# Kernel optimization log

Hardware: AMD Instinct MI355X
Metric: run time of the kernel (lower is better)

The kernel has to match this reference:

```python
import jax, jax.numpy as jnp
import numpy as np

B, S, D = 1, 2048, 4096
H, KVH, HD = 32, 8, 128
GROUPS = H // KVH  # 4
SCALE = HD ** -0.5
NEG = jnp.finfo(jnp.float32).min


def rotate_half(x):
    x1 = x[..., : x.shape[-1] // 2]
    x2 = x[..., x.shape[-1] // 2:]
    return jnp.concatenate((-x2, x1), axis=-1)


def setup_inputs() -> dict:
    key = jax.random.key(0)
    ks = jax.random.split(key, 8)
    return {
        "hidden_states": jax.random.normal(ks[0], (B, S, D), dtype=jnp.float32),
        "cos": jax.random.uniform(ks[1], (B, S, HD), dtype=jnp.float32),
        "sin": jax.random.uniform(ks[2], (B, S, HD), dtype=jnp.float32),
        "attention_mask": jnp.ones((B, S), dtype=bool),
        "wq": jax.random.normal(ks[3], (D, H * HD), dtype=jnp.float32) * 0.02,
        "wk": jax.random.normal(ks[4], (D, KVH * HD), dtype=jnp.float32) * 0.02,
        "wv": jax.random.normal(ks[5], (D, KVH * HD), dtype=jnp.float32) * 0.02,
        "wo": jax.random.normal(ks[6], (H * HD, D), dtype=jnp.float32) * 0.02,
    }


def reference(hidden_states, cos, sin, attention_mask, wq, wk, wv, wo):
    b, s, _ = hidden_states.shape
    # projections -> (B,S,heads,head_dim)
    q = (hidden_states @ wq).reshape(b, s, H, HD)
    k = (hidden_states @ wk).reshape(b, s, KVH, HD)
    v = (hidden_states @ wv).reshape(b, s, KVH, HD)
    # RoPE (cos/sin unsqueezed at head axis)
    c = cos[:, :, None, :]
    si = sin[:, :, None, :]
    q = q * c + rotate_half(q) * si
    k = k * c + rotate_half(k) * si
    # GQA: repeat kv heads (cache_index=0, max_len==S -> cache write is identity)
    k = jnp.repeat(k, GROUPS, axis=2)
    v = jnp.repeat(v, GROUPS, axis=2)
    # mask: causal AND padding; bias 0 / -inf
    causal = jnp.tril(jnp.ones((s, s), dtype=bool))[None, None]  # (1,1,S,S)
    mask = causal & attention_mask[:, None, None, :]  # (B,1,S,S)
    bias = jnp.where(mask, 0.0, NEG).astype(hidden_states.dtype)
    # scores (B,H,S,S)
    scores = jnp.einsum("bqhd,bkhd->bhqk", q, k) * SCALE + bias
    attn = jax.nn.softmax(scores, axis=-1)
    out = jnp.einsum("bhqk,bkhd->bqhd", attn, v).reshape(b, s, H * HD)
    return out @ wo
```

## Files before the change

### kernel.cpp

```cpp
#include <hip/hip_runtime.h>
#include <hip/hip_bf16.h>

#define SEQ   2048
#define DM    4096
#define NH    32
#define NKVH  8
#define HD    128
#define NQKV  6144
#define KOFF  4096
#define VOFF  5120
#define QLD   5120
#define SCALE 0.08838834764831845f

typedef __attribute__((ext_vector_type(4))) float f32x4;
typedef __attribute__((ext_vector_type(8))) short short8;

__device__ __forceinline__ unsigned short f2bf(float f) {
  union { float f; unsigned int u; } v; v.f = f;
  unsigned int r = v.u + 0x7FFF + ((v.u >> 16) & 1);
  return (unsigned short)(r >> 16);
}
__device__ __forceinline__ float bf2f(unsigned short b) {
  union { unsigned int u; float f; } v; v.u = ((unsigned int)b) << 16;
  return v.f;
}

__device__ __forceinline__ void gld16(const unsigned short* g, unsigned short* l) {
  __builtin_amdgcn_global_load_lds(
      (const __attribute__((address_space(1))) unsigned int*)g,
      (__attribute__((address_space(3))) unsigned int*)l, 16, 0, 0);
}

__global__ __launch_bounds__(256) void prep(const float* __restrict__ hs,
                                            const float* __restrict__ wq,
                                            const float* __restrict__ wk,
                                            const float* __restrict__ wv,
                                            const float* __restrict__ wo,
                                            unsigned short* __restrict__ hsb,
                                            unsigned short* __restrict__ wqkvT,
                                            unsigned short* __restrict__ woT) {
  __shared__ unsigned short t2[64][72];
  const int bxg = blockIdx.x;
  const int tid = threadIdx.x;
  if (bxg < 8192) {
    size_t i = ((size_t)bxg * 256 + tid) * 4;
    float4 v = *(const float4*)(hs + i);
    ushort4 o;
    o.x = f2bf(v.x); o.y = f2bf(v.y); o.z = f2bf(v.z); o.w = f2bf(v.w);
    *(ushort4*)(hsb + i) = o;
    return;
  }
  const int b  = bxg - 8192;
  const int bx = b % 160;
  const int k0 = (b / 160) * 64;
  const float* W; unsigned short* out; int N, n0, row_off;
  if (bx < 64)      { W = wq; out = wqkvT; N = 4096; n0 = bx * 64;        row_off = 0;    }
  else if (bx < 80) { W = wk; out = wqkvT; N = 1024; n0 = (bx - 64) * 64; row_off = 4096; }
  else if (bx < 96) { W = wv; out = wqkvT; N = 1024; n0 = (bx - 80) * 64; row_off = 5120; }
  else              { W = wo; out = woT;   N = 4096; n0 = (bx - 96) * 64; row_off = 0;    }

  const int n  = tid & 63;
  const int q  = tid >> 6;
#pragma unroll
  for (int i = 0; i < 4; ++i) {
    const int kq = (i * 4 + q) * 4;
    float f0 = W[(size_t)(k0 + kq + 0) * N + n0 + n];
    float f1 = W[(size_t)(k0 + kq + 1) * N + n0 + n];
    float f2 = W[(size_t)(k0 + kq + 2) * N + n0 + n];
    float f3 = W[(size_t)(k0 + kq + 3) * N + n0 + n];
    ushort4 u; u.x = f2bf(f0); u.y = f2bf(f1); u.z = f2bf(f2); u.w = f2bf(f3);
    *(ushort4*)&t2[n][kq] = u;
  }
  __syncthreads();

  const int sn = tid >> 3;
  const int c8 = (tid & 7) * 8;
#pragma unroll
  for (int i = 0; i < 2; ++i) {
    const int nn = sn + i * 32;
    short8 v = *(const short8*)&t2[nn][c8];
    *(short8*)&out[(size_t)(row_off + n0 + nn) * DM + k0 + c8] = v;
  }
}

__global__ __launch_bounds__(256) void gemm_bt(const unsigned short* __restrict__ A,
                                               const unsigned short* __restrict__ Bt,
                                               void* __restrict__ C,
                                               unsigned short* __restrict__ vt,
                                               int M, int N, int K, int ldc, int c_fp32) {
  __shared__ unsigned short As[2][128 * 32];
  __shared__ unsigned short Bs[2][128 * 32];
  const int tid  = threadIdx.x;
  const int m0   = blockIdx.y * 128;
  const int n0   = blockIdx.x * 128;
  const int w    = tid >> 6;
  const int lane = tid & 63;
  const int l16  = lane & 15;
  const int quad = lane >> 4;
  const int wr   = (w >> 1) * 64;
  const int wc   = (w & 1) * 64;

  f32x4 acc[4][4];
#pragma unroll
  for (int i = 0; i < 4; ++i)
#pragma unroll
    for (int j = 0; j < 4; ++j) acc[i][j] = (f32x4){0.f, 0.f, 0.f, 0.f};

  const int sr  = lane >> 2;
  const int pb  = lane & 3;
  const int sws = (sr & 3) ^ ((sr >> 2) & 3);
  const int kb  = ((pb ^ sws) << 3);
  const unsigned short* ga0 = A  + (size_t)(m0 + w * 16 + sr) * K + kb;
  const unsigned short* ga1 = A  + (size_t)(m0 + 64 + w * 16 + sr) * K + kb;
  const unsigned short* gb0 = Bt + (size_t)(n0 + w * 16 + sr) * K + kb;
  const unsigned short* gb1 = Bt + (size_t)(n0 + 64 + w * 16 + sr) * K + kb;
  const int lofs0 = (w * 16) * 32;
  const int lofs1 = (64 + w * 16) * 32;

  const int swf  = (l16 & 3) ^ ((l16 >> 2) & 3);
  const int fcol = ((quad ^ swf) << 3);

  gld16(ga0, &As[0][lofs0]);
  gld16(ga1, &As[0][lofs1]);
  gld16(gb0, &Bs[0][lofs0]);
  gld16(gb1, &Bs[0][lofs1]);

  int p = 0;
  for (int k0 = 0; k0 < K; k0 += 32) {
    __syncthreads();
    if (k0 + 32 < K) {
      gld16(ga0 + k0 + 32, &As[p ^ 1][lofs0]);
      gld16(ga1 + k0 + 32, &As[p ^ 1][lofs1]);
      gld16(gb0 + k0 + 32, &Bs[p ^ 1][lofs0]);
      gld16(gb1 + k0 + 32, &Bs[p ^ 1][lofs1]);
    }
    short8 af[4], bfr[4];
#pragma unroll
    for (int mt = 0; mt < 4; ++mt)
      af[mt] = *(const short8*)&As[p][(wr + mt * 16 + l16) * 32 + fcol];
#pragma unroll
    for (int nt = 0; nt < 4; ++nt)
      bfr[nt] = *(const short8*)&Bs[p][(wc + nt * 16 + l16) * 32 + fcol];
#pragma unroll
    for (int mt = 0; mt < 4; ++mt)
#pragma unroll
      for (int nt = 0; nt < 4; ++nt)
        acc[mt][nt] = __builtin_amdgcn_mfma_f32_16x16x32_bf16(af[mt], bfr[nt], acc[mt][nt], 0, 0, 0);
    p ^= 1;
  }

  if (vt && n0 >= VOFF) {
#pragma unroll
    for (int mt = 0; mt < 4; ++mt)
#pragma unroll
      for (int nt = 0; nt < 4; ++nt) {
        int col  = (n0 - VOFF) + wc + nt * 16 + l16;
        int row0 = m0 + wr + mt * 16 + quad * 4;
        ushort4 ov;
        ov.x = f2bf(acc[mt][nt][0]); ov.y = f2bf(acc[mt][nt][1]);
        ov.z = f2bf(acc[mt][nt][2]); ov.w = f2bf(acc[mt][nt][3]);
        *(ushort4*)&vt[(size_t)col * SEQ + row0] = ov;
      }
  } else if (c_fp32) {
    float* Cf = (float*)C;
#pragma unroll
    for (int mt = 0; mt < 4; ++mt)
#pragma unroll
      for (int nt = 0; nt < 4; ++nt) {
        int col = n0 + wc + nt * 16 + l16;
#pragma unroll
        for (int r = 0; r < 4; ++r)
          Cf[(size_t)(m0 + wr + mt * 16 + quad * 4 + r) * ldc + col] = acc[mt][nt][r];
      }
  } else {
    unsigned short* Cb = (unsigned short*)C;
#pragma unroll
    for (int mt = 0; mt < 4; ++mt)
#pragma unroll
      for (int nt = 0; nt < 4; ++nt) {
        int col = n0 + wc + nt * 16 + l16;
#pragma unroll
        for (int r = 0; r < 4; ++r)
          Cb[(size_t)(m0 + wr + mt * 16 + quad * 4 + r) * ldc + col] = f2bf(acc[mt][nt][r]);
      }
  }
}

__global__ __launch_bounds__(256) void rope_kernel(unsigned short* __restrict__ QKV,
                                                   const float* __restrict__ cosb,
                                                   const float* __restrict__ sinb) {
  int idx = blockIdx.x * 256 + threadIdx.x;
  int i = idx & 63;
  int h = (idx >> 6) % 40;
  int s = idx / 2560;
  size_t base = (size_t)s * QLD + (size_t)h * 128;
  float q1 = bf2f(QKV[base + i]);
  float q2 = bf2f(QKV[base + i + 64]);
  float c1 = cosb[s * 128 + i],      s1 = sinb[s * 128 + i];
  float c2 = cosb[s * 128 + i + 64], s2 = sinb[s * 128 + i + 64];
  QKV[base + i]      = f2bf(q1 * c1 - q2 * s1);
  QKV[base + i + 64] = f2bf(q2 * c2 + q1 * s2);
}

__global__ __launch_bounds__(256) void flash_attn(const unsigned short* __restrict__ QKV,
                                                  const unsigned short* __restrict__ Vt_g,
                                                  unsigned short* __restrict__ AO) {
  __shared__ unsigned short Ks[64 * 136];
  __shared__ unsigned short Vs[128 * 72];
  __shared__ unsigned short Ps[4][32 * 68];

  const int h   = blockIdx.x;
  const int qt  = (int)gridDim.y - 1 - (int)blockIdx.y;
  const int kvh = h >> 2;
  const int tid  = threadIdx.x;
  const int w    = tid >> 6;
  const int lane = tid & 63;
  const int l16  = lane & 15;
  const int quad = lane >> 4;
  const int q0   = qt * 128;
  const int qrow_w = q0 + w * 32;

  short8 qf[2][4];
#pragma unroll
  for (int ntq = 0; ntq < 2; ++ntq) {
    const unsigned short* qp = QKV + (size_t)(qrow_w + ntq * 16 + l16) * QLD + h * HD + quad * 8;
#pragma unroll
    for (int ks = 0; ks < 4; ++ks) qf[ntq][ks] = *(const short8*)(qp + ks * 32);
  }

  f32x4 o[8][2];
#pragma unroll
  for (int i = 0; i < 8; ++i) { o[i][0] = (f32x4){0,0,0,0}; o[i][1] = (f32x4){0,0,0,0}; }
  float m_i[2] = {-3.0e38f, -3.0e38f}, l_i[2] = {0.f, 0.f};

  const int kr = tid >> 2, kcol0 = (tid & 3) * 32;
  const int vr = tid >> 1, vcol0 = (tid & 1) * 32;
  const unsigned short* kbase = QKV + KOFF + (size_t)kvh * HD + kcol0;
  const unsigned short* vbase = Vt_g + ((size_t)kvh * HD + vr) * SEQ + vcol0;

  const int nch = qt * 2 + 2;

  short8 kv[4], vv[4];
#pragma unroll
  for (int u = 0; u < 4; ++u) kv[u] = *(const short8*)(kbase + (size_t)kr * QLD + u * 8);
#pragma unroll
  for (int u = 0; u < 4; ++u) vv[u] = *(const short8*)(vbase + u * 8);

  for (int c = 0; c < nch; ++c) {
    const int kc = c * 64;
    __builtin_amdgcn_s_barrier();
#pragma unroll
    for (int u = 0; u < 4; ++u) *(short8*)&Ks[kr * 136 + kcol0 + u * 8] = kv[u];
#pragma unroll
    for (int u = 0; u < 4; ++u) *(short8*)&Vs[vr * 72 + vcol0 + u * 8] = vv[u];
    if (c + 1 < nch) {
      const int kn = kc + 64;
#pragma unroll
      for (int u = 0; u < 4; ++u) kv[u] = *(const short8*)(kbase + (size_t)(kn + kr) * QLD + u * 8);
#pragma unroll
      for (int u = 0; u < 4; ++u) vv[u] = *(const short8*)(vbase + kn + u * 8);
    }
    asm volatile("s_waitcnt lgkmcnt(0)" ::: "memory");
    __builtin_amdgcn_s_barrier();

    if (kc <= qrow_w + 31) {
      f32x4 st[4][2];
#pragma unroll
      for (int mt = 0; mt < 4; ++mt) { st[mt][0] = (f32x4){0,0,0,0}; st[mt][1] = (f32x4){0,0,0,0}; }
      __builtin_amdgcn_s_setprio(1);
#pragma unroll
      for (int ks = 0; ks < 4; ++ks)
#pragma unroll
        for (int mt = 0; mt < 4; ++mt) {
          short8 ak = *(const short8*)&Ks[(mt * 16 + l16) * 136 + ks * 32 + quad * 8];
          st[mt][0] = __builtin_amdgcn_mfma_f32_16x16x32_bf16(ak, qf[0][ks], st[mt][0], 0, 0, 0);
          st[mt][1] = __builtin_amdgcn_mfma_f32_16x16x32_bf16(ak, qf[1][ks], st[mt][1], 0, 0, 0);
        }
      __builtin_amdgcn_s_setprio(0);

      float sc[4][2][4];
#pragma unroll
      for (int mt = 0; mt < 4; ++mt)
#pragma unroll
        for (int ntq = 0; ntq < 2; ++ntq) {
          int qr = qrow_w + ntq * 16 + l16;
#pragma unroll
          for (int r = 0; r < 4; ++r) {
            int key = kc + mt * 16 + quad * 4 + r;
            float v = st[mt][ntq][r] * SCALE;
            sc[mt][ntq][r] = (key <= qr) ? v : -__builtin_inff();
          }
        }
      float mx[2] = {-__builtin_inff(), -__builtin_inff()};
#pragma unroll
      for (int mt = 0; mt < 4; ++mt)
#pragma unroll
        for (int ntq = 0; ntq < 2; ++ntq)
#pragma unroll
          for (int r = 0; r < 4; ++r) mx[ntq] = fmaxf(mx[ntq], sc[mt][ntq][r]);
#pragma unroll
      for (int ntq = 0; ntq < 2; ++ntq) {
        mx[ntq] = fmaxf(mx[ntq], __shfl_xor(mx[ntq], 16, 64));
        mx[ntq] = fmaxf(mx[ntq], __shfl_xor(mx[ntq], 32, 64));
      }
      float al[2], mn[2];
#pragma unroll
      for (int ntq = 0; ntq < 2; ++ntq) {
        mn[ntq] = fmaxf(m_i[ntq], mx[ntq]);
        al[ntq] = __expf(m_i[ntq] - mn[ntq]);
        m_i[ntq] = mn[ntq];
      }

      float rs[2] = {0.f, 0.f};
      unsigned short* psw = &Ps[w][0];
#pragma unroll
      for (int mt = 0; mt < 4; ++mt)
#pragma unroll
        for (int ntq = 0; ntq < 2; ++ntq) {
          float p0 = __expf(sc[mt][ntq][0] - mn[ntq]);
          float p1 = __expf(sc[mt][ntq][1] - mn[ntq]);
          float p2 = __expf(sc[mt][ntq][2] - mn[ntq]);
          float p3 = __expf(sc[mt][ntq][3] - mn[ntq]);
          rs[ntq] += (p0 + p1) + (p2 + p3);
          ushort4 pk; pk.x = f2bf(p0); pk.y = f2bf(p1); pk.z = f2bf(p2); pk.w = f2bf(p3);
          *(ushort4*)&psw[(ntq * 16 + l16) * 68 + mt * 16 + quad * 4] = pk;
        }
#pragma unroll
      for (int ntq = 0; ntq < 2; ++ntq) {
        rs[ntq] += __shfl_xor(rs[ntq], 16, 64);
        rs[ntq] += __shfl_xor(rs[ntq], 32, 64);
        l_i[ntq] = l_i[ntq] * al[ntq] + rs[ntq];
      }
#pragma unroll
      for (int i = 0; i < 8; ++i) {
        o[i][0][0] *= al[0]; o[i][0][1] *= al[0]; o[i][0][2] *= al[0]; o[i][0][3] *= al[0];
        o[i][1][0] *= al[1]; o[i][1][1] *= al[1]; o[i][1][2] *= al[1]; o[i][1][3] *= al[1];
      }

#pragma unroll
      for (int ks = 0; ks < 2; ++ks) {
        short8 bp[2];
#pragma unroll
        for (int ntq = 0; ntq < 2; ++ntq) {
          union { ushort4 h[2]; short8 v; } u;
          const unsigned short* pp = &psw[(ntq * 16 + l16) * 68 + ks * 32 + quad * 8];
          u.h[0] = *(const ushort4*)(pp);
          u.h[1] = *(const ushort4*)(pp + 4);
          bp[ntq] = u.v;
        }
        __builtin_amdgcn_s_setprio(1);
#pragma unroll
        for (int mt = 0; mt < 8; ++mt) {
          short8 av = *(const short8*)&Vs[(mt * 16 + l16) * 72 + ks * 32 + quad * 8];
          o[mt][0] = __builtin_amdgcn_mfma_f32_16x16x32_bf16(av, bp[0], o[mt][0], 0, 0, 0);
          o[mt][1] = __builtin_amdgcn_mfma_f32_16x16x32_bf16(av, bp[1], o[mt][1], 0, 0, 0);
        }
        __builtin_amdgcn_s_setprio(0);
      }
    }
  }

  float inv[2] = {1.0f / l_i[0], 1.0f / l_i[1]};
#pragma unroll
  for (int mt = 0; mt < 8; ++mt)
#pragma unroll
    for (int ntq = 0; ntq < 2; ++ntq) {
      int qr = qrow_w + ntq * 16 + l16;
      int col = h * HD + mt * 16 + quad * 4;
      ushort4 ov;
      ov.x = f2bf(o[mt][ntq][0] * inv[ntq]);
      ov.y = f2bf(o[mt][ntq][1] * inv[ntq]);
      ov.z = f2bf(o[mt][ntq][2] * inv[ntq]);
      ov.w = f2bf(o[mt][ntq][3] * inv[ntq]);
      *(ushort4*)&AO[(size_t)qr * DM + col] = ov;
    }
}

extern "C" void kernel_launch(void* const* d_in, const int* in_sizes, int n_in,
                              void* d_out, int out_size, void* d_ws, size_t ws_size,
                              hipStream_t stream) {
  const float* hs   = (const float*)d_in[0];
  const float* cosb = (const float*)d_in[1];
  const float* sinb = (const float*)d_in[2];
  const float* wq = (const float*)d_in[4];
  const float* wk = (const float*)d_in[5];
  const float* wv = (const float*)d_in[6];
  const float* wo = (const float*)d_in[7];
  float* out = (float*)d_out;

  char* ws = (char*)d_ws;
  unsigned short* hsb   = (unsigned short*)(ws);
  unsigned short* wqkvT = (unsigned short*)(ws + (16u << 20));
  unsigned short* woT   = (unsigned short*)(ws + (64u << 20));
  unsigned short* qkv   = (unsigned short*)(ws + (96u << 20));
  unsigned short* ao    = (unsigned short*)(ws + (116u << 20));
  unsigned short* Vt_g  = (unsigned short*)(ws + (132u << 20));

  prep<<<8192 + 160 * 64, 256, 0, stream>>>(hs, wq, wk, wv, wo, hsb, wqkvT, woT);
  gemm_bt<<<dim3(NQKV / 128, SEQ / 128), 256, 0, stream>>>(hsb, wqkvT, qkv, Vt_g, SEQ, NQKV, DM, QLD, 0);
  rope_kernel<<<20480, 256, 0, stream>>>(qkv, cosb, sinb);
  flash_attn<<<dim3(NH, SEQ / 128), 256, 0, stream>>>(qkv, Vt_g, ao);
  gemm_bt<<<dim3(DM / 128, SEQ / 128), 256, 0, stream>>>(ao, woT, out, nullptr, SEQ, DM, DM, DM, 1);
}
```

Baseline: 526.1 us.

## Fuse Q RoPE into attention, skip masking on full chunks, lazy softmax rescale

Q rotary embedding is now applied in registers inside the attention kernel, so the standalone rope kernel only processes K heads. Fully unmasked key chunks skip the causal comparison. The running max and output rescale are updated only when the chunk max exceeds the old max by more than a threshold, which avoids most exp and multiply work. The cost is larger unnormalised probabilities and extra cos/sin reads per attention block.

```diff
diff --git a/kernel.cpp b/kernel.cpp
--- a/kernel.cpp
+++ b/kernel.cpp
@@ -186,14 +186,14 @@
   }
 }
 
-__global__ __launch_bounds__(256) void rope_kernel(unsigned short* __restrict__ QKV,
-                                                   const float* __restrict__ cosb,
-                                                   const float* __restrict__ sinb) {
+__global__ __launch_bounds__(256) void rope_k(unsigned short* __restrict__ QKV,
+                                              const float* __restrict__ cosb,
+                                              const float* __restrict__ sinb) {
   int idx = blockIdx.x * 256 + threadIdx.x;
-  int i = idx & 63;
-  int h = (idx >> 6) % 40;
-  int s = idx / 2560;
-  size_t base = (size_t)s * QLD + (size_t)h * 128;
+  int i  = idx & 63;
+  int hk = (idx >> 6) & 7;
+  int s  = idx >> 9;
+  size_t base = (size_t)s * QLD + KOFF + (size_t)hk * 128;
   float q1 = bf2f(QKV[base + i]);
   float q2 = bf2f(QKV[base + i + 64]);
   float c1 = cosb[s * 128 + i],      s1 = sinb[s * 128 + i];
@@ -204,6 +204,8 @@
 
 __global__ __launch_bounds__(256) void flash_attn(const unsigned short* __restrict__ QKV,
                                                   const unsigned short* __restrict__ Vt_g,
+                                                  const float* __restrict__ cosb,
+                                                  const float* __restrict__ sinb,
                                                   unsigned short* __restrict__ AO) {
   __shared__ unsigned short Ks[64 * 136];
   __shared__ unsigned short Vs[128 * 72];
@@ -223,9 +225,25 @@
   short8 qf[2][4];
 #pragma unroll
   for (int ntq = 0; ntq < 2; ++ntq) {
-    const unsigned short* qp = QKV + (size_t)(qrow_w + ntq * 16 + l16) * QLD + h * HD + quad * 8;
+    const int s_row = qrow_w + ntq * 16 + l16;
+    const unsigned short* qp = QKV + (size_t)s_row * QLD + h * HD + quad * 8;
 #pragma unroll
     for (int ks = 0; ks < 4; ++ks) qf[ntq][ks] = *(const short8*)(qp + ks * 32);
+    const float* cb = cosb + (size_t)s_row * 128 + quad * 8;
+    const float* sb = sinb + (size_t)s_row * 128 + quad * 8;
+#pragma unroll
+    for (int ks = 0; ks < 2; ++ks) {
+#pragma unroll
+      for (int e = 0; e < 8; ++e) {
+        int d = ks * 32 + e;
+        float f1 = bf2f((unsigned short)qf[ntq][ks][e]);
+        float f2 = bf2f((unsigned short)qf[ntq][ks + 2][e]);
+        float c1 = cb[d],      s1v = sb[d];
+        float c2 = cb[d + 64], s2v = sb[d + 64];
+        qf[ntq][ks][e]     = (short)f2bf(f1 * c1 - f2 * s1v);
+        qf[ntq][ks + 2][e] = (short)f2bf(f2 * c2 + f1 * s2v);
+      }
+    }
   }
 
   f32x4 o[8][2];
@@ -279,18 +297,28 @@
       __builtin_amdgcn_s_setprio(0);
 
       float sc[4][2][4];
-#pragma unroll
-      for (int mt = 0; mt < 4; ++mt)
-#pragma unroll
-        for (int ntq = 0; ntq < 2; ++ntq) {
-          int qr = qrow_w + ntq * 16 + l16;
-#pragma unroll
-          for (int r = 0; r < 4; ++r) {
-            int key = kc + mt * 16 + quad * 4 + r;
-            float v = st[mt][ntq][r] * SCALE;
-            sc[mt][ntq][r] = (key <= qr) ? v : -__builtin_inff();
+      const bool fullch = (kc + 64 <= qrow_w);
+      if (fullch) {
+#pragma unroll
+        for (int mt = 0; mt < 4; ++mt)
+#pragma unroll
+          for (int ntq = 0; ntq < 2; ++ntq)
+#pragma unroll
+            for (int r = 0; r < 4; ++r) sc[mt][ntq][r] = st[mt][ntq][r] * SCALE;
+      } else {
+#pragma unroll
+        for (int mt = 0; mt < 4; ++mt)
+#pragma unroll
+          for (int ntq = 0; ntq < 2; ++ntq) {
+            int qr = qrow_w + ntq * 16 + l16;
+#pragma unroll
+            for (int r = 0; r < 4; ++r) {
+              int key = kc + mt * 16 + quad * 4 + r;
+              float v = st[mt][ntq][r] * SCALE;
+              sc[mt][ntq][r] = (key <= qr) ? v : -__builtin_inff();
+            }
           }
-        }
+      }
       float mx[2] = {-__builtin_inff(), -__builtin_inff()};
 #pragma unroll
       for (int mt = 0; mt < 4; ++mt)
@@ -303,12 +331,22 @@
         mx[ntq] = fmaxf(mx[ntq], __shfl_xor(mx[ntq], 16, 64));
         mx[ntq] = fmaxf(mx[ntq], __shfl_xor(mx[ntq], 32, 64));
       }
-      float al[2], mn[2];
-#pragma unroll
-      for (int ntq = 0; ntq < 2; ++ntq) {
-        mn[ntq] = fmaxf(m_i[ntq], mx[ntq]);
-        al[ntq] = __expf(m_i[ntq] - mn[ntq]);
-        m_i[ntq] = mn[ntq];
+
+      bool upd = (mx[0] > m_i[0] + 8.f) || (mx[1] > m_i[1] + 8.f);
+      if (__any(upd ? 1 : 0)) {
+        float al[2];
+#pragma unroll
+        for (int ntq = 0; ntq < 2; ++ntq) {
+          float mn = fmaxf(m_i[ntq], mx[ntq]);
+          al[ntq] = __expf(m_i[ntq] - mn);
+          m_i[ntq] = mn;
+          l_i[ntq] *= al[ntq];
+        }
+#pragma unroll
+        for (int i = 0; i < 8; ++i) {
+          o[i][0][0] *= al[0]; o[i][0][1] *= al[0]; o[i][0][2] *= al[0]; o[i][0][3] *= al[0];
+          o[i][1][0] *= al[1]; o[i][1][1] *= al[1]; o[i][1][2] *= al[1]; o[i][1][3] *= al[1];
+        }
       }
 
       float rs[2] = {0.f, 0.f};
@@ -317,10 +355,10 @@
       for (int mt = 0; mt < 4; ++mt)
 #pragma unroll
         for (int ntq = 0; ntq < 2; ++ntq) {
-          float p0 = __expf(sc[mt][ntq][0] - mn[ntq]);
-          float p1 = __expf(sc[mt][ntq][1] - mn[ntq]);
-          float p2 = __expf(sc[mt][ntq][2] - mn[ntq]);
-          float p3 = __expf(sc[mt][ntq][3] - mn[ntq]);
+          float p0 = __expf(sc[mt][ntq][0] - m_i[ntq]);
+          float p1 = __expf(sc[mt][ntq][1] - m_i[ntq]);
+          float p2 = __expf(sc[mt][ntq][2] - m_i[ntq]);
+          float p3 = __expf(sc[mt][ntq][3] - m_i[ntq]);
           rs[ntq] += (p0 + p1) + (p2 + p3);
           ushort4 pk; pk.x = f2bf(p0); pk.y = f2bf(p1); pk.z = f2bf(p2); pk.w = f2bf(p3);
           *(ushort4*)&psw[(ntq * 16 + l16) * 68 + mt * 16 + quad * 4] = pk;
@@ -329,12 +367,7 @@
       for (int ntq = 0; ntq < 2; ++ntq) {
         rs[ntq] += __shfl_xor(rs[ntq], 16, 64);
         rs[ntq] += __shfl_xor(rs[ntq], 32, 64);
-        l_i[ntq] = l_i[ntq] * al[ntq] + rs[ntq];
-      }
-#pragma unroll
-      for (int i = 0; i < 8; ++i) {
-        o[i][0][0] *= al[0]; o[i][0][1] *= al[0]; o[i][0][2] *= al[0]; o[i][0][3] *= al[0];
-        o[i][1][0] *= al[1]; o[i][1][1] *= al[1]; o[i][1][2] *= al[1]; o[i][1][3] *= al[1];
+        l_i[ntq] += rs[ntq];
       }
 
 #pragma unroll
@@ -398,7 +431,7 @@
 
   prep<<<8192 + 160 * 64, 256, 0, stream>>>(hs, wq, wk, wv, wo, hsb, wqkvT, woT);
   gemm_bt<<<dim3(NQKV / 128, SEQ / 128), 256, 0, stream>>>(hsb, wqkvT, qkv, Vt_g, SEQ, NQKV, DM, QLD, 0);
-  rope_kernel<<<20480, 256, 0, stream>>>(qkv, cosb, sinb);
-  flash_attn<<<dim3(NH, SEQ / 128), 256, 0, stream>>>(qkv, Vt_g, ao);
+  rope_k<<<4096, 256, 0, stream>>>(qkv, cosb, sinb);
+  flash_attn<<<dim3(NH, SEQ / 128), 256, 0, stream>>>(qkv, Vt_g, cosb, sinb, ao);
   gemm_bt<<<dim3(DM / 128, SEQ / 128), 256, 0, stream>>>(ao, woT, out, nullptr, SEQ, DM, DM, DM, 1);
 }
```

New measurement: 524.0 us. Within noise of the previous version (-0.4%).
